# Optimization experiments

Measured on AMD Instinct MI355X. Metric: run time of the kernel, lower is better.

## Reference

```python
import jax, jax.numpy as jnp
import numpy as np

B = 16384
G = 2048   # granule_cell_count
N = 512    # ca3_cell_count
DT = 0.5   # integration_timestep
STEPS = 5  # ca3_attractor_steps
A_REC = 0.02   # recovery_time_constant
B_SUB = 0.2    # subthreshold_coupling
C_RESET = -55.0  # spike_reset_voltage
D_AHP = 4.0      # after_hyperpolarization_jump
CONN_P = 0.1


def setup_inputs() -> dict:
    key = jax.random.key(0)
    k1, k2, k3, k4 = jax.random.split(key, 4)
    dg_query_spikes = (jax.random.uniform(k1, (B, G)) < 0.1).astype(jnp.float32)
    W_mossy = 0.05 * jax.random.normal(k2, (N, G), dtype=jnp.float32)
    mask = (jax.random.uniform(k3, (N, N)) < CONN_P).astype(jnp.float32)
    W_rec = mask * jax.random.uniform(k4, (N, N)) * 0.1
    W_rec = W_rec * (1.0 - jnp.eye(N, dtype=jnp.float32))  # zero diagonal
    v0 = jnp.full((N,), -65.0, dtype=jnp.float32)
    u0 = jnp.full((N,), 0.2 * -65.0, dtype=jnp.float32)
    return {"dg_query_spikes": dg_query_spikes, "W_mossy": W_mossy,
            "W_rec": W_rec, "v0": v0, "u0": u0}


def _izhikevich_step(v, u, I):
    # Euler step of the Izhikevich neuron model, per original torch code.
    dv = 0.04 * v * v + 5.0 * v + 140.0 - u + I
    du = A_REC * (B_SUB * v - u)
    v = v + dv * DT
    u = u + du * DT
    spike = (v >= 30.0).astype(v.dtype)
    v = jnp.where(spike > 0, jnp.asarray(C_RESET, v.dtype), v)
    u = u + spike * D_AHP
    v = jnp.clip(v, -90.0, 30.0)
    return v, u, spike


def reference(dg_query_spikes, W_mossy, W_rec, v0, u0):
    # query_current = Linear(dg) * 10.0  -> [B, N]
    query_current = (dg_query_spikes @ W_mossy.T) * 10.0
    v = jnp.broadcast_to(v0, (B, N))
    u = jnp.broadcast_to(u0, (B, N))
    spike = jnp.zeros((B, N), dtype=jnp.float32)
    for _ in range(STEPS):  # fixed small unrolled recurrence
        # torch.mv(W_rec, spikes) batched: [B,N] @ [N,N]^T
        recurrent_current = (v >= 30.0).astype(jnp.float32) @ W_rec.T
        total_current = query_current + recurrent_current
        v, u, spike = _izhikevich_step(v, u, total_current)
    return spike
```

## Files before the change

kernel.cpp:

```cpp
#include <hip/hip_runtime.h>
#include <cstdint>
#include <cstddef>


typedef __attribute__((ext_vector_type(8))) short bf16x8;
typedef __attribute__((ext_vector_type(8))) unsigned short u16x8;
typedef __attribute__((ext_vector_type(4))) float f32x4;
typedef __attribute__((ext_vector_type(4))) unsigned int u32x4;

constexpr int Bn = 16384, Gn = 2048, Nn = 512;
constexpr size_t B_BYTES    = (size_t)256 * Nn * 16;
constexpr size_t BITS_BYTES = (size_t)Bn * 256;
constexpr unsigned int CAP = 700000;
constexpr size_t OFF_BITS = B_BYTES;
constexpr size_t OFF_THR  = OFF_BITS + BITS_BYTES;
constexpr size_t OFF_CNT  = OFF_THR + 64;
constexpr size_t OFF_LIST = OFF_CNT + 64;
constexpr size_t WS_NEED  = OFF_LIST + (size_t)CAP * 4;
constexpr float DELTA = 0.125f;

__device__ __forceinline__ unsigned short f2bf(float x) {
  uint32_t u = __builtin_bit_cast(uint32_t, x);
  u += 0x7FFFu + ((u >> 16) & 1u);
  return (unsigned short)(u >> 16);
}

__device__ __forceinline__ void glds16(const void* g, const void* l) {
  __builtin_amdgcn_global_load_lds(
      (const __attribute__((address_space(1))) unsigned int*)g,
      (__attribute__((address_space(3))) unsigned int*)l, 16, 0, 0);
}

__device__ __forceinline__ float izhi5(float I, float vi, float ui) {
#pragma clang fp contract(off)
  float v = vi, u = ui, spk = 0.0f;
#pragma unroll
  for (int st = 0; st < 5; ++st) {
    float dv = 0.04f * v * v + 5.0f * v + 140.0f - u + I;
    float du = 0.02f * (0.2f * v - u);
    v = v + dv * 0.5f;
    u = u + du * 0.5f;
    spk = (v >= 30.0f) ? 1.0f : 0.0f;
    if (spk > 0.0f) v = -55.0f;
    u = u + spk * 4.0f;
    v = fminf(fmaxf(v, -90.0f), 30.0f);
  }
  return spk;
}

__global__ void calibrate(const float* __restrict__ v0, const float* __restrict__ u0,
                          float* __restrict__ thr, unsigned int* __restrict__ cnt) {
  const int l = (int)threadIdx.x;
  if (l == 0) cnt[0] = 0u;
  const float vi = v0[0], ui = u0[0];
  const float X0 = -45.0f;
  const float step = 90.0f / 64.0f;
  const float s = izhi5(X0 + step * (float)l, vi, ui);
  const float sp = __shfl_up(s, 1);
  unsigned long long m = __ballot((l > 0) && (s != sp));
  float t[2] = {1e30f, 1e30f};
#pragma unroll
  for (int k = 0; k < 2; ++k) {
    if (!m) break;
    const int i = __ffsll((long long)m) - 1;
    m &= m - 1;
    float lo = X0 + step * (float)(i - 1);
    float hi = X0 + step * (float)i;
    for (int rr = 0; rr < 3; ++rr) {
      const float st2 = (hi - lo) / 64.0f;
      const float ss = izhi5(lo + st2 * (float)l, vi, ui);
      const float s0 = __shfl(ss, 0);
      const unsigned long long mm = __ballot(ss != s0);
      const int ii = mm ? (__ffsll((long long)mm) - 1) : 64;
      hi = lo + st2 * (float)ii;
      lo = lo + st2 * (float)(ii - 1);
    }
    t[k] = 0.5f * (lo + hi);
  }
  if (l == 0) { thr[0] = t[0]; thr[1] = t[1]; }
}

__launch_bounds__(256)
__global__ void prep_W(const float* __restrict__ Wm, unsigned short* __restrict__ Bb) {
  const int n  = (int)blockIdx.x;
  const int gi = (int)threadIdx.x;
  const float* src = Wm + (size_t)n * Gn + gi * 8;
  u16x8 h0;
#pragma unroll
  for (int e = 0; e < 8; ++e) h0[e] = f2bf(src[e]);
  *reinterpret_cast<u16x8*>(reinterpret_cast<char*>(Bb) +
                            ((size_t)gi * Nn + n) * 16) = h0;
}

__launch_bounds__(256)
__global__ void prep_bits(const float* __restrict__ dg, uint32_t* __restrict__ bits) {
  __shared__ uint32_t nib[32 * 576];
  const int t  = (int)threadIdx.x;
  const int r0 = (int)blockIdx.x * 32;
#pragma unroll 4
  for (int i = 0; i < 64; ++i) {
    const int idx = i * 256 + t;
    const int row = idx >> 9;
    const int col = idx & 511;
    const float4 x = *reinterpret_cast<const float4*>(
        dg + (size_t)(r0 + row) * Gn + col * 4);
    uint32_t n = (x.x != 0.0f ? 1u : 0u) | (x.y != 0.0f ? 2u : 0u) |
                 (x.z != 0.0f ? 4u : 0u) | (x.w != 0.0f ? 8u : 0u);
    nib[row * 576 + col + (col >> 3)] = n;
  }
  __syncthreads();
#pragma unroll
  for (int i = 0; i < 8; ++i) {
    const int oidx = i * 256 + t;
    const int r   = oidx >> 6;
    const int kh  = (oidx >> 4) & 3;
    const int ktq = oidx & 15;
    uint32_t by[4];
#pragma unroll
    for (int q = 0; q < 4; ++q) {
      const int kt = ktq * 4 + q;
      const int cp = kt * 8 + kh * 2 + kt;
      const uint32_t ne = nib[r * 576 + cp];
      const uint32_t no = nib[r * 576 + cp + 1];
      by[q] = ne | (no << 4);
    }
    const uint32_t w = by[0] | (by[1] << 8) | (by[2] << 16) | (by[3] << 24);
    bits[(size_t)(r0 + r) * 64 + kh * 16 + ktq] = w;
  }
}

__launch_bounds__(256, 2)
__global__ void gemm_bits(const uint32_t* __restrict__ bits, const char* __restrict__ Bb,
                          const float* __restrict__ thr,
                          unsigned int* __restrict__ cnt,
                          unsigned int* __restrict__ list,
                          float* __restrict__ out) {
  __shared__ __align__(16) char lds[65536];
  const int t = (int)threadIdx.x;
  const int bx0 = (int)blockIdx.x;
  const int bx  = (bx0 & 7) * 64 + (bx0 >> 3);
  const int mt = bx >> 3, nt = bx & 7;
  const int m0 = mt * 256, n0 = nt * 64;

  const uint32_t bbase = (uint32_t)((((t >> 6) * Nn) + n0 + (t & 63)) * 16);
  const uint32_t bdst0 = (uint32_t)(t * 16);

  const int l  = t & 63, w = t >> 6;
  const int lr = l & 15, kh = l >> 4;

  uint32_t abase[4];
#pragma unroll
  for (int mf = 0; mf < 4; ++mf)
    abase[mf] = (uint32_t)((m0 + w * 64 + mf * 16 + lr) * 256 + kh * 64);
  uint32_t boff[4];
#pragma unroll
  for (int nf = 0; nf < 4; ++nf)
    boff[nf] = (uint32_t)((kh * 64 + nf * 16 + lr) * 16);

  f32x4 acc[4][4];
#pragma unroll
  for (int i = 0; i < 4; ++i)
#pragma unroll
    for (int j = 0; j < 4; ++j)
      acc[i][j] = (f32x4){0.0f, 0.0f, 0.0f, 0.0f};

  const char* bitsc = (const char*)bits;

  for (int c = 0; c < 4; ++c) {
    if (c) __syncthreads();
#pragma unroll
    for (int o = 0; o < 16; ++o)
      glds16(Bb + (size_t)c * 524288 + o * 32768 + bbase,
             &lds[o * 4096 + bdst0]);
    u32x4 ab[4];
#pragma unroll
    for (int mf = 0; mf < 4; ++mf)
      ab[mf] = *reinterpret_cast<const u32x4*>(bitsc + abase[mf] + c * 16);
    __syncthreads();

#pragma unroll
    for (int ktl = 0; ktl < 16; ++ktl) {
      bf16x8 bq[4];
#pragma unroll
      for (int nf = 0; nf < 4; ++nf)
        bq[nf] = *reinterpret_cast<const bf16x8*>(&lds[ktl * 4096 + boff[nf]]);
#pragma unroll
      for (int mf = 0; mf < 4; ++mf) {
        const uint32_t e = ab[mf][ktl >> 2];
        const uint32_t b = e >> ((ktl & 3) * 8);
        u32x4 aw;
        aw.x = (b & 1u)   * 0x3F80u     | (b & 2u)   * 0x1FC00000u;
        aw.y = (b & 4u)   * 0xFE0u      | (b & 8u)   * 0x07F00000u;
        aw.z = (b & 16u)  * 0x3F8u      | (b & 32u)  * 0x01FC0000u;
        aw.w = (b & 64u)  * 0xFEu       | (b & 128u) * 0x007F0000u;
        const bf16x8 af = __builtin_bit_cast(bf16x8, aw);
#pragma unroll
        for (int nf = 0; nf < 4; ++nf)
          acc[mf][nf] = __builtin_amdgcn_mfma_f32_16x16x32_bf16(
              af, bq[nf], acc[mf][nf], 0, 0, 0);
      }
    }
  }

  const float I5 = thr[0], I4 = thr[1];
#pragma unroll
  for (int nf = 0; nf < 4; ++nf) {
    const int ncol = n0 + nf * 16 + lr;
#pragma unroll
    for (int mf = 0; mf < 4; ++mf) {
      const int mrow = m0 + w * 64 + mf * 16 + kh * 4;
#pragma unroll
      for (int r = 0; r < 4; ++r) {
        const float I = acc[mf][nf][r] * 10.0f;
        const float sp = (I > I5 && I < I4) ? 1.0f : 0.0f;
        out[(size_t)(mrow + r) * Nn + ncol] = sp;
        if (fabsf(I - I5) < DELTA || fabsf(I - I4) < DELTA) {
          const unsigned int idx = atomicAdd(cnt, 1u);
          if (idx < CAP)
            list[idx] = (unsigned int)(mrow + r) * (unsigned int)Nn + (unsigned int)ncol;
        }
      }
    }
  }
}

__launch_bounds__(256)
__global__ void fixup(const float* __restrict__ dg, const float* __restrict__ Wm,
                      const float* __restrict__ v0, const float* __restrict__ u0,
                      const unsigned int* __restrict__ cnt,
                      const unsigned int* __restrict__ list,
                      float* __restrict__ out) {
#pragma clang fp contract(off)
  const unsigned int n = min(cnt[0], CAP);
  const unsigned int wid0   = (blockIdx.x * blockDim.x + threadIdx.x) >> 6;
  const unsigned int nwaves = (gridDim.x * blockDim.x) >> 6;
  const int l = (int)(threadIdx.x & 63);
  for (unsigned int i = wid0; i < n; i += nwaves) {
    const unsigned int e = list[i];
    const unsigned int m = e >> 9, nn = e & 511u;
    const float* dr = dg + (size_t)m * Gn;
    const float* wr = Wm + (size_t)nn * Gn;
    float acc = 0.0f;
#pragma unroll
    for (int j = 0; j < 8; ++j) {
      const int g = j * 256 + l * 4;
      const float4 d = *reinterpret_cast<const float4*>(dr + g);
      const float4 w = *reinterpret_cast<const float4*>(wr + g);
      acc += (d.x != 0.0f) ? w.x : 0.0f;
      acc += (d.y != 0.0f) ? w.y : 0.0f;
      acc += (d.z != 0.0f) ? w.z : 0.0f;
      acc += (d.w != 0.0f) ? w.w : 0.0f;
    }
#pragma unroll
    for (int off = 32; off > 0; off >>= 1) acc += __shfl_down(acc, off);
    if (l == 0)
      out[(size_t)m * Nn + nn] = izhi5(acc * 10.0f, v0[nn], u0[nn]);
  }
}

constexpr int ROWS = 32, TG = 16, NCHUNK = Gn / 32;

__launch_bounds__(512, 2)
__global__ void ca3_sparse_kernel(const float* __restrict__ dg,
                                  const float* __restrict__ Wm,
                                  const float* __restrict__ v0,
                                  const float* __restrict__ u0,
                                  float* __restrict__ out) {
#pragma clang fp contract(off)
  __shared__ float    lds_w[TG * Nn];
  __shared__ uint32_t lds_bits[ROWS][NCHUNK];
  const int t    = (int)threadIdx.x;
  const int row0 = (int)blockIdx.x * ROWS;
  {
    const int r  = t >> 4;
    const int c0 = (t & 15) * 4;
    const float* p = dg + (size_t)(row0 + r) * Gn + (size_t)c0 * 32;
#pragma unroll
    for (int cc = 0; cc < 4; ++cc) {
      uint32_t bb = 0;
#pragma unroll
      for (int i = 0; i < 8; ++i) {
        float4 x = reinterpret_cast<const float4*>(p + cc * 32)[i];
        bb |= (x.x != 0.0f ? 1u : 0u) << (i * 4 + 0);
        bb |= (x.y != 0.0f ? 1u : 0u) << (i * 4 + 1);
        bb |= (x.z != 0.0f ? 1u : 0u) << (i * 4 + 2);
        bb |= (x.w != 0.0f ? 1u : 0u) << (i * 4 + 3);
      }
      lds_bits[r][c0 + cc] = bb;
    }
  }
  float acc[ROWS];
#pragma unroll
  for (int r = 0; r < ROWS; ++r) acc[r] = 0.0f;
  for (int gt = 0; gt < Gn / TG; ++gt) {
    __syncthreads();
    {
      const int k  = t & 3;
      const int nb = t >> 2;
#pragma unroll
      for (int pq = 0; pq < 4; ++pq) {
        const int n = pq * 128 + nb;
        const float4 w4 = *reinterpret_cast<const float4*>(
            Wm + (size_t)n * Gn + gt * TG + k * 4);
        lds_w[(k * 4 + 0) * Nn + n] = w4.x;
        lds_w[(k * 4 + 1) * Nn + n] = w4.y;
        lds_w[(k * 4 + 2) * Nn + n] = w4.z;
        lds_w[(k * 4 + 3) * Nn + n] = w4.w;
      }
    }
    __syncthreads();
    const int shift = (gt & 1) * 16;
#pragma unroll
    for (int r = 0; r < ROWS; ++r) {
      uint32_t b = (lds_bits[r][gt >> 1] >> shift) & 0xFFFFu;
      b = __builtin_amdgcn_readfirstlane(b);
      while (b) {
        const int g0 = __builtin_ctz(b);
        const uint32_t b1 = b & (b - 1);
        const int g1 = __builtin_ctz(b1 | 0x8000u);
        const uint32_t b2 = b1 & (b1 - 1);
        const int g2 = __builtin_ctz(b2 | 0x8000u);
        const uint32_t b3 = b2 & (b2 - 1);
        const int g3 = __builtin_ctz(b3 | 0x8000u);
        float x0 = lds_w[g0 * Nn + t];
        float x1 = lds_w[g1 * Nn + t];
        float x2 = lds_w[g2 * Nn + t];
        float x3 = lds_w[g3 * Nn + t];
        x1 = (b1 != 0u) ? x1 : 0.0f;
        x2 = (b2 != 0u) ? x2 : 0.0f;
        x3 = (b3 != 0u) ? x3 : 0.0f;
        acc[r] += x0; acc[r] += x1; acc[r] += x2; acc[r] += x3;
        b = b3 & (b3 - 1);
      }
    }
  }
  const float vi = v0[t];
  const float ui = u0[t];
#pragma unroll
  for (int r = 0; r < ROWS; ++r) {
    out[(size_t)(row0 + r) * Nn + t] = izhi5(acc[r] * 10.0f, vi, ui);
  }
}

extern "C" void kernel_launch(void* const* d_in, const int* in_sizes, int n_in,
                              void* d_out, int out_size, void* d_ws, size_t ws_size,
                              hipStream_t stream) {
  const float* dg = (const float*)d_in[0];
  const float* Wm = (const float*)d_in[1];
  const float* v0 = (const float*)d_in[3];
  const float* u0 = (const float*)d_in[4];
  float* out = (float*)d_out;

  if (ws_size < WS_NEED) {
    hipLaunchKernelGGL(ca3_sparse_kernel, dim3(Bn / ROWS), dim3(512), 0, stream,
                       dg, Wm, v0, u0, out);
    return;
  }
  char* base = (char*)d_ws;
  unsigned short* Bb = (unsigned short*)base;
  uint32_t* bits     = (uint32_t*)(base + OFF_BITS);
  float* thr         = (float*)(base + OFF_THR);
  unsigned int* cnt  = (unsigned int*)(base + OFF_CNT);
  unsigned int* list = (unsigned int*)(base + OFF_LIST);

  hipLaunchKernelGGL(calibrate, dim3(1), dim3(64), 0, stream, v0, u0, thr, cnt);
  hipLaunchKernelGGL(prep_W, dim3(512), dim3(256), 0, stream, Wm, Bb);
  hipLaunchKernelGGL(prep_bits, dim3(512), dim3(256), 0, stream, dg, bits);
  hipLaunchKernelGGL(gemm_bits, dim3(512), dim3(256), 0, stream,
                     bits, (const char*)Bb, thr, cnt, list, out);
  hipLaunchKernelGGL(fixup, dim3(512), dim3(256), 0, stream,
                     dg, Wm, v0, u0, cnt, list, out);
}
```

Before: 124.5 us.

## Permute bit and weight layouts so GEMM reads operands directly without LDS

Both prep kernels now write the bit-packed query matrix and the bf16 mossy weights in an MFMA-fragment-permuted layout. This lets the GEMM load each operand straight from global memory with coalesced 16-byte loads and no LDS staging. Dropping the shared-memory buffer and its barriers also allows smaller 64x128 tiles, 1024 blocks and higher occupancy (launch bounds 4). The cost is that B fragments are re-read from L2 by every block with no LDS reuse across waves.

Result: faster. 121.8 us (-2.2%).

```diff
diff --git a/kernel.cpp b/kernel.cpp
--- a/kernel.cpp
+++ b/kernel.cpp
@@ -9,8 +9,8 @@
 typedef __attribute__((ext_vector_type(4))) unsigned int u32x4;
 
 constexpr int Bn = 16384, Gn = 2048, Nn = 512;
-constexpr size_t B_BYTES    = (size_t)256 * Nn * 16;
-constexpr size_t BITS_BYTES = (size_t)Bn * 256;
+constexpr size_t B_BYTES    = (size_t)64 * 32 * 4 * 16 * 16;
+constexpr size_t BITS_BYTES = (size_t)1024 * 4 * 4 * 16 * 16;
 constexpr unsigned int CAP = 700000;
 constexpr size_t OFF_BITS = B_BYTES;
 constexpr size_t OFF_THR  = OFF_BITS + BITS_BYTES;
@@ -23,12 +23,6 @@
   uint32_t u = __builtin_bit_cast(uint32_t, x);
   u += 0x7FFFu + ((u >> 16) & 1u);
   return (unsigned short)(u >> 16);
-}
-
-__device__ __forceinline__ void glds16(const void* g, const void* l) {
-  __builtin_amdgcn_global_load_lds(
-      (const __attribute__((address_space(1))) unsigned int*)g,
-      (__attribute__((address_space(3))) unsigned int*)l, 16, 0, 0);
 }
 
 __device__ __forceinline__ float izhi5(float I, float vi, float ui) {
@@ -81,19 +75,20 @@
 }
 
 __launch_bounds__(256)
-__global__ void prep_W(const float* __restrict__ Wm, unsigned short* __restrict__ Bb) {
+__global__ void prep_W(const float* __restrict__ Wm, char* __restrict__ Bperm) {
   const int n  = (int)blockIdx.x;
   const int gi = (int)threadIdx.x;
   const float* src = Wm + (size_t)n * Gn + gi * 8;
   u16x8 h0;
 #pragma unroll
   for (int e = 0; e < 8; ++e) h0[e] = f2bf(src[e]);
-  *reinterpret_cast<u16x8*>(reinterpret_cast<char*>(Bb) +
-                            ((size_t)gi * Nn + n) * 16) = h0;
+  const int kt = gi >> 2, kh = gi & 3;
+  const size_t dst = (size_t)kt * 32768 + (n >> 4) * 1024 + kh * 256 + (n & 15) * 16;
+  *reinterpret_cast<u16x8*>(Bperm + dst) = h0;
 }
 
 __launch_bounds__(256)
-__global__ void prep_bits(const float* __restrict__ dg, uint32_t* __restrict__ bits) {
+__global__ void prep_bits(const float* __restrict__ dg, uint32_t* __restrict__ bitsP) {
   __shared__ uint32_t nib[32 * 576];
   const int t  = (int)threadIdx.x;
   const int r0 = (int)blockIdx.x * 32;
@@ -124,91 +119,74 @@
       const uint32_t no = nib[r * 576 + cp + 1];
       by[q] = ne | (no << 4);
     }
-    const uint32_t w = by[0] | (by[1] << 8) | (by[2] << 16) | (by[3] << 24);
-    bits[(size_t)(r0 + r) * 64 + kh * 16 + ktq] = w;
-  }
-}
-
-__launch_bounds__(256, 2)
-__global__ void gemm_bits(const uint32_t* __restrict__ bits, const char* __restrict__ Bb,
+    const uint32_t wd = by[0] | (by[1] << 8) | (by[2] << 16) | (by[3] << 24);
+    const int row = r0 + r;
+    const int rowgrp = row >> 4, rl = row & 15;
+    const int ktg = ktq >> 2;
+    bitsP[rowgrp * 1024 + ktg * 256 + kh * 64 + rl * 4 + (ktq & 3)] = wd;
+  }
+}
+
+__launch_bounds__(256, 4)
+__global__ void gemm_perm(const char* __restrict__ bitsP, const char* __restrict__ Bperm,
                           const float* __restrict__ thr,
                           unsigned int* __restrict__ cnt,
                           unsigned int* __restrict__ list,
                           float* __restrict__ out) {
-  __shared__ __align__(16) char lds[65536];
   const int t = (int)threadIdx.x;
   const int bx0 = (int)blockIdx.x;
-  const int bx  = (bx0 & 7) * 64 + (bx0 >> 3);
-  const int mt = bx >> 3, nt = bx & 7;
-  const int m0 = mt * 256, n0 = nt * 64;
-
-  const uint32_t bbase = (uint32_t)((((t >> 6) * Nn) + n0 + (t & 63)) * 16);
-  const uint32_t bdst0 = (uint32_t)(t * 16);
+  const int bx  = (bx0 & 7) * 128 + (bx0 >> 3);
+  const int mt = bx >> 2, nt = bx & 3;
+  const int m0 = mt * 64, n0 = nt * 128;
 
   const int l  = t & 63, w = t >> 6;
   const int lr = l & 15, kh = l >> 4;
-
-  uint32_t abase[4];
-#pragma unroll
-  for (int mf = 0; mf < 4; ++mf)
-    abase[mf] = (uint32_t)((m0 + w * 64 + mf * 16 + lr) * 256 + kh * 64);
-  uint32_t boff[4];
-#pragma unroll
-  for (int nf = 0; nf < 4; ++nf)
-    boff[nf] = (uint32_t)((kh * 64 + nf * 16 + lr) * 16);
-
-  f32x4 acc[4][4];
-#pragma unroll
-  for (int i = 0; i < 4; ++i)
-#pragma unroll
-    for (int j = 0; j < 4; ++j)
-      acc[i][j] = (f32x4){0.0f, 0.0f, 0.0f, 0.0f};
-
-  const char* bitsc = (const char*)bits;
-
-  for (int c = 0; c < 4; ++c) {
-    if (c) __syncthreads();
-#pragma unroll
-    for (int o = 0; o < 16; ++o)
-      glds16(Bb + (size_t)c * 524288 + o * 32768 + bbase,
-             &lds[o * 4096 + bdst0]);
+  const int n0w = n0 + w * 32;
+  const int ng0 = n0w >> 4;
+
+  const char* bpw = Bperm + (size_t)ng0 * 1024 + kh * 256 + lr * 16;
+  const char* apw = bitsP + (size_t)(m0 >> 4) * 4096 + kh * 256 + lr * 16;
+
+  f32x4 acc[4][2];
+#pragma unroll
+  for (int i = 0; i < 4; ++i) {
+    acc[i][0] = (f32x4){0.0f, 0.0f, 0.0f, 0.0f};
+    acc[i][1] = (f32x4){0.0f, 0.0f, 0.0f, 0.0f};
+  }
+
+  for (int ktg = 0; ktg < 4; ++ktg) {
     u32x4 ab[4];
 #pragma unroll
     for (int mf = 0; mf < 4; ++mf)
-      ab[mf] = *reinterpret_cast<const u32x4*>(bitsc + abase[mf] + c * 16);
-    __syncthreads();
-
+      ab[mf] = *reinterpret_cast<const u32x4*>(apw + mf * 4096 + ktg * 1024);
 #pragma unroll
     for (int ktl = 0; ktl < 16; ++ktl) {
-      bf16x8 bq[4];
-#pragma unroll
-      for (int nf = 0; nf < 4; ++nf)
-        bq[nf] = *reinterpret_cast<const bf16x8*>(&lds[ktl * 4096 + boff[nf]]);
+      const int kt = ktg * 16 + ktl;
+      const bf16x8 bq0 = *reinterpret_cast<const bf16x8*>(bpw + (size_t)kt * 32768);
+      const bf16x8 bq1 = *reinterpret_cast<const bf16x8*>(bpw + (size_t)kt * 32768 + 1024);
 #pragma unroll
       for (int mf = 0; mf < 4; ++mf) {
         const uint32_t e = ab[mf][ktl >> 2];
         const uint32_t b = e >> ((ktl & 3) * 8);
         u32x4 aw;
-        aw.x = (b & 1u)   * 0x3F80u     | (b & 2u)   * 0x1FC00000u;
-        aw.y = (b & 4u)   * 0xFE0u      | (b & 8u)   * 0x07F00000u;
-        aw.z = (b & 16u)  * 0x3F8u      | (b & 32u)  * 0x01FC0000u;
-        aw.w = (b & 64u)  * 0xFEu       | (b & 128u) * 0x007F0000u;
+        aw.x = (b & 1u)   * 0x3F80u | (b & 2u)   * 0x1FC00000u;
+        aw.y = (b & 4u)   * 0xFE0u  | (b & 8u)   * 0x07F00000u;
+        aw.z = (b & 16u)  * 0x3F8u  | (b & 32u)  * 0x01FC0000u;
+        aw.w = (b & 64u)  * 0xFEu   | (b & 128u) * 0x007F0000u;
         const bf16x8 af = __builtin_bit_cast(bf16x8, aw);
-#pragma unroll
-        for (int nf = 0; nf < 4; ++nf)
-          acc[mf][nf] = __builtin_amdgcn_mfma_f32_16x16x32_bf16(
-              af, bq[nf], acc[mf][nf], 0, 0, 0);
+        acc[mf][0] = __builtin_amdgcn_mfma_f32_16x16x32_bf16(af, bq0, acc[mf][0], 0, 0, 0);
+        acc[mf][1] = __builtin_amdgcn_mfma_f32_16x16x32_bf16(af, bq1, acc[mf][1], 0, 0, 0);
       }
     }
   }
 
   const float I5 = thr[0], I4 = thr[1];
 #pragma unroll
-  for (int nf = 0; nf < 4; ++nf) {
-    const int ncol = n0 + nf * 16 + lr;
+  for (int nf = 0; nf < 2; ++nf) {
+    const int ncol = n0w + nf * 16 + lr;
 #pragma unroll
     for (int mf = 0; mf < 4; ++mf) {
-      const int mrow = m0 + w * 64 + mf * 16 + kh * 4;
+      const int mrow = m0 + mf * 16 + kh * 4;
 #pragma unroll
       for (int r = 0; r < 4; ++r) {
         const float I = acc[mf][nf][r] * 10.0f;
@@ -357,17 +335,17 @@
     return;
   }
   char* base = (char*)d_ws;
-  unsigned short* Bb = (unsigned short*)base;
-  uint32_t* bits     = (uint32_t*)(base + OFF_BITS);
+  char* Bperm        = base;
+  uint32_t* bitsP    = (uint32_t*)(base + OFF_BITS);
   float* thr         = (float*)(base + OFF_THR);
   unsigned int* cnt  = (unsigned int*)(base + OFF_CNT);
   unsigned int* list = (unsigned int*)(base + OFF_LIST);
 
   hipLaunchKernelGGL(calibrate, dim3(1), dim3(64), 0, stream, v0, u0, thr, cnt);
-  hipLaunchKernelGGL(prep_W, dim3(512), dim3(256), 0, stream, Wm, Bb);
-  hipLaunchKernelGGL(prep_bits, dim3(512), dim3(256), 0, stream, dg, bits);
-  hipLaunchKernelGGL(gemm_bits, dim3(512), dim3(256), 0, stream,
-                     bits, (const char*)Bb, thr, cnt, list, out);
+  hipLaunchKernelGGL(prep_W, dim3(512), dim3(256), 0, stream, Wm, Bperm);
+  hipLaunchKernelGGL(prep_bits, dim3(512), dim3(256), 0, stream, dg, bitsP);
+  hipLaunchKernelGGL(gemm_perm, dim3(1024), dim3(256), 0, stream,
+                     (const char*)bitsP, (const char*)Bperm, thr, cnt, list, out);
   hipLaunchKernelGGL(fixup, dim3(512), dim3(256), 0, stream,
                      dg, Wm, v0, u0, cnt, list, out);
 }
```
